# Kernel tuning notes

Hardware: AMD Instinct MI355X
Metric: run time of the kernel (lower is better)

Reference implementation:

```python
import jax, jax.numpy as jnp
import numpy as np
from jax import lax

N, L, D, F = 16, 512, 256, 256
KW = 3
EPS = 1e-5


def setup_inputs() -> dict:
    key = jax.random.key(0)
    ks = jax.random.split(key, 12)
    return {
        "x": jax.random.normal(ks[0], (N, L, D), jnp.float32),
        "conv1_w": jax.random.normal(ks[1], (F, D, KW), jnp.float32) * 0.05,
        "conv1_b": jnp.zeros((F,), jnp.float32),
        "ln1_g": jnp.ones((F,), jnp.float32),
        "ln1_b": jnp.zeros((F,), jnp.float32),
        "conv2_w": jax.random.normal(ks[2], (F, F, KW), jnp.float32) * 0.05,
        "conv2_b": jnp.zeros((F,), jnp.float32),
        "ln2_g": jnp.ones((F,), jnp.float32),
        "ln2_b": jnp.zeros((F,), jnp.float32),
        "lin_w": jax.random.normal(ks[3], (F, 1), jnp.float32) * 0.05,
        "lin_b": jnp.zeros((1,), jnp.float32),
        "target": jax.random.randint(ks[4], (N, L), 1, 8, jnp.int32),
        "mel_max_length": 4096,
    }


def _layernorm(h, g, b):
    m = jnp.mean(h, axis=-1, keepdims=True)
    v = jnp.var(h, axis=-1, keepdims=True)
    return (h - m) * lax.rsqrt(v + EPS) * g + b


def _conv1d(h, w, b):
    # h: [N, L, C_in]; w: [C_out, C_in, K]; 'same' padding=1 for K=3
    y = lax.conv_general_dilated(h.transpose(0, 2, 1), w, (1,), [(1, 1)],
                                 dimension_numbers=("NCH", "OIH", "NCH"))
    return (y + b[None, :, None]).transpose(0, 2, 1)


def _duration_predictor(x, c1w, c1b, g1, b1, c2w, c2b, g2, b2, lw, lb):
    h = jax.nn.relu(_layernorm(_conv1d(x, c1w, c1b), g1, b1))
    h = jax.nn.relu(_layernorm(_conv1d(h, c2w, c2b), g2, b2))
    return jax.nn.relu(h @ lw + lb)[..., 0]  # [N, L]


def _length_regulate(x, dur, T):
    # Equivalent to one-hot alignment @ x, done as a duration-indexed gather.
    cum = jnp.cumsum(dur, axis=-1)                       # [N, L]
    t = jnp.arange(T, dtype=cum.dtype)                   # [T]
    idx = jax.vmap(lambda c: jnp.searchsorted(c, t, side="right"))(cum)  # [N, T]
    valid = t[None, :] < cum[:, -1:]                     # [N, T]
    out = jnp.take_along_axis(x, jnp.clip(idx, 0, x.shape[1] - 1)[:, :, None], axis=1)
    return jnp.where(valid[..., None], out, jnp.zeros((), x.dtype))


def reference(x, conv1_w, conv1_b, ln1_g, ln1_b, conv2_w, conv2_b, ln2_g, ln2_b,
              lin_w, lin_b, target, mel_max_length):
    dpo = _duration_predictor(x, conv1_w, conv1_b, ln1_g, ln1_b,
                              conv2_w, conv2_b, ln2_g, ln2_b, lin_w, lin_b)
    out = _length_regulate(x, target, mel_max_length)    # [N, mel_max_length, D]
    return (out, dpo)
```

## Files before the change

kernel.cpp:

```cpp
#include <hip/hip_runtime.h>
#include <hip/hip_bf16.h>

using u16 = unsigned short;
typedef __bf16 bf16x8 __attribute__((ext_vector_type(8)));
typedef float f32x4 __attribute__((ext_vector_type(4)));

#define N_B   16
#define L_S   512
#define D_F   256
#define T_MEL 4096
#define M_TOT (N_B * L_S)
#define OUT_ELEMS ((size_t)N_B * T_MEL * D_F)
#define H1_ELEMS  ((size_t)M_TOT * D_F)
#define WP_ELEMS  (24 * 8192)
#define TBLK 128

__device__ __forceinline__ u16 f2bf(float f) {
  __hip_bfloat16 h = __float2bfloat16(f);
  return *(u16*)&h;
}

__device__ __forceinline__ bf16x8 pack8(float4 v0, float4 v1) {
  union { bf16x8 h; u16 u[8]; } r;
  r.u[0] = f2bf(v0.x); r.u[1] = f2bf(v0.y); r.u[2] = f2bf(v0.z); r.u[3] = f2bf(v0.w);
  r.u[4] = f2bf(v1.x); r.u[5] = f2bf(v1.y); r.u[6] = f2bf(v1.z); r.u[7] = f2bf(v1.w);
  return r.h;
}

__global__ __launch_bounds__(256)
void pack_kernel(const float* __restrict__ w1, const float* __restrict__ w2,
                 u16* __restrict__ wp1, u16* __restrict__ wp2) {
  int o   = (int)blockIdx.x * 256 + (int)threadIdx.x;
  int s   = o >> 13;
  int rem = o & 8191;
  int f   = rem >> 5;
  int ki  = rem & 31;
  int d   = ((s & 7) << 5) + ki;
  int tap = s >> 3;
  int src = f * 768 + d * 3 + tap;
  wp1[o] = f2bf(w1[src]);
  wp2[o] = f2bf(w2[src]);
}

template<int STAGE>
__global__ __launch_bounds__(512)
void conv_ln_kernel(const float* __restrict__ Xf,
                    const u16*  __restrict__ Xh,
                    const u16*  __restrict__ Wp,
                    const float* __restrict__ cb,  const float* __restrict__ lgm,
                    const float* __restrict__ lbt, const float* __restrict__ lw,
                    const float* __restrict__ lb,  u16* __restrict__ Hout,
                    float* __restrict__ dpo)
{
  __shared__ __align__(16) u16 As[34 * 264 + 8];
  __shared__ __align__(16) u16 Bs[2 * 8192];
  __shared__ float sBias[256], sG[256], sB[256], sLw[256];
  __shared__ float redS[2][4][16], redQ[2][4][16];

  const int t = threadIdx.x;
  if (t < 256) {
    sBias[t] = cb[t];
    sG[t]    = lgm[t];
    sB[t]    = lbt[t];
    if (STAGE == 2) sLw[t] = lw[t];
  }

  const int m0   = (int)blockIdx.x * 32;
  const int n    = m0 >> 9;
  const int l0   = m0 & 511;
  const int wave = t >> 6, lane = t & 63;
  const int cs   = wave & 3;
  const int rh   = wave >> 2;
  const int wc   = cs * 64;
  const int rh16 = rh * 16;
  const int p    = lane & 15, q = lane >> 4;

  for (int c = t; c < 1088; c += 512) {
    int row  = c >> 5;
    int col8 = c & 31;
    int l    = l0 + row - 1;
    uint4 val;
    if ((unsigned)l < 512u) {
      if (STAGE == 1) {
        const float* src = Xf + (((size_t)((n << 9) + l)) << 8) + (col8 << 3);
        float4 v0 = *(const float4*)src;
        float4 v1 = *(const float4*)(src + 4);
        bf16x8 pk = pack8(v0, v1);
        __builtin_memcpy(&val, &pk, 16);
      } else {
        val = *(const uint4*)(Xh + (((size_t)((n << 9) + l)) << 8) + (col8 << 3));
      }
    } else {
      val = make_uint4(0u, 0u, 0u, 0u);
    }
    *(uint4*)(As + row * 264 + (col8 << 3)) = val;
  }
  {
    uint4 r0 = *(const uint4*)(Wp + (t << 3));
    uint4 r1 = *(const uint4*)(Wp + ((t + 512) << 3));
    *(uint4*)(Bs + (t << 3))         = r0;
    *(uint4*)(Bs + ((t + 512) << 3)) = r1;
  }
  __syncthreads();

  f32x4 acc[4];
  #pragma unroll
  for (int i = 0; i < 4; i++) acc[i] = (f32x4){0.f, 0.f, 0.f, 0.f};

  for (int s = 0; s < 24; s++) {
    const int cur = s & 1;
    uint4 r0, r1;
    if (s < 23) {
      const u16* src = Wp + ((size_t)(s + 1) << 13);
      r0 = *(const uint4*)(src + (t << 3));
      r1 = *(const uint4*)(src + ((t + 512) << 3));
    }
    {
      const u16* bs = Bs + (cur << 13);
      const int tap = s >> 3, dbase = (s & 7) << 5;
      bf16x8 af = *(const bf16x8*)(As + (rh16 + p + tap) * 264 + dbase + (q << 3));
      #pragma unroll
      for (int ct = 0; ct < 4; ct++) {
        bf16x8 bfr = *(const bf16x8*)(bs + ((wc + ct * 16 + p) << 5) + (q << 3));
        acc[ct] = __builtin_amdgcn_mfma_f32_16x16x32_bf16(af, bfr, acc[ct], 0, 0, 0);
      }
    }
    if (s < 23) {
      __syncthreads();
      *(uint4*)(Bs + ((cur ^ 1) << 13) + (t << 3))         = r0;
      *(uint4*)(Bs + ((cur ^ 1) << 13) + ((t + 512) << 3)) = r1;
      __syncthreads();
    }
  }

  float s0[4] = {0,0,0,0}, s1[4] = {0,0,0,0};
  #pragma unroll
  for (int ct = 0; ct < 4; ct++) {
    float bias = sBias[wc + ct * 16 + p];
    #pragma unroll
    for (int j = 0; j < 4; j++) {
      float v = acc[ct][j] + bias;
      acc[ct][j] = v;
      s0[j] += v;
      s1[j] += v * v;
    }
  }
  #pragma unroll
  for (int m = 1; m <= 8; m <<= 1) {
    #pragma unroll
    for (int j = 0; j < 4; j++) {
      s0[j] += __shfl_xor(s0[j], m);
      s1[j] += __shfl_xor(s1[j], m);
    }
  }
  if (p == 0) {
    #pragma unroll
    for (int j = 0; j < 4; j++) {
      redS[rh][cs][q * 4 + j] = s0[j];
      redQ[rh][cs][q * 4 + j] = s1[j];
    }
  }
  __syncthreads();
  float mean[4], rstd[4];
  #pragma unroll
  for (int j = 0; j < 4; j++) {
    int r = q * 4 + j;
    float S = redS[rh][0][r] + redS[rh][1][r] + redS[rh][2][r] + redS[rh][3][r];
    float Q = redQ[rh][0][r] + redQ[rh][1][r] + redQ[rh][2][r] + redQ[rh][3][r];
    float mu  = S * (1.0f / 256.0f);
    float var = Q * (1.0f / 256.0f) - mu * mu;
    mean[j] = mu;
    rstd[j] = rsqrtf(var + 1e-5f);
  }

  if (STAGE == 1) {
    #pragma unroll
    for (int ct = 0; ct < 4; ct++) {
      int c = wc + ct * 16 + p;
      float gg = sG[c], bb = sB[c];
      #pragma unroll
      for (int j = 0; j < 4; j++) {
        float v = (acc[ct][j] - mean[j]) * rstd[j] * gg + bb;
        v = fmaxf(v, 0.0f);
        Hout[(size_t)(m0 + rh16 + q * 4 + j) * 256 + c] = f2bf(v);
      }
    }
  } else {
    float ls[4] = {0,0,0,0};
    #pragma unroll
    for (int ct = 0; ct < 4; ct++) {
      int c = wc + ct * 16 + p;
      float gg = sG[c], bb = sB[c], ww = sLw[c];
      #pragma unroll
      for (int j = 0; j < 4; j++) {
        float v = (acc[ct][j] - mean[j]) * rstd[j] * gg + bb;
        v = fmaxf(v, 0.0f);
        ls[j] += v * ww;
      }
    }
    #pragma unroll
    for (int m = 1; m <= 8; m <<= 1) {
      #pragma unroll
      for (int j = 0; j < 4; j++) ls[j] += __shfl_xor(ls[j], m);
    }
    __syncthreads();
    if (p == 0) {
      #pragma unroll
      for (int j = 0; j < 4; j++) redS[rh][cs][q * 4 + j] = ls[j];
    }
    __syncthreads();
    if (t < 32) {
      int r2 = t >> 4, ri = t & 15;
      float dv = fmaxf(redS[r2][0][ri] + redS[r2][1][ri] +
                       redS[r2][2][ri] + redS[r2][3][ri] + lb[0], 0.0f);
      dpo[m0 + t] = dv;
    }
  }
}

__global__ __launch_bounds__(256)
void lr_kernel(const float* __restrict__ X, const int* __restrict__ tgt,
               float* __restrict__ out) {
  __shared__ int c[L_S];
  __shared__ int sidx[TBLK];
  const int t  = threadIdx.x;
  const int n  = blockIdx.x >> 5;
  const int t0 = (blockIdx.x & 31) * TBLK;

  c[t]       = tgt[n * L_S + t];
  c[t + 256] = tgt[n * L_S + t + 256];
  __syncthreads();
  for (int off = 1; off < L_S; off <<= 1) {
    int v0 = (t >= off) ? c[t - off] : 0;
    int i1 = t + 256;
    int v1 = (i1 >= off) ? c[i1 - off] : 0;
    __syncthreads();
    c[t]  += v0;
    c[i1] += v1;
    __syncthreads();
  }
  const int total = c[L_S - 1];
  if (t < TBLK) {
    int tt = t0 + t;
    int lo = 0, hi = L_S;
    while (lo < hi) {
      int mid = (lo + hi) >> 1;
      if (c[mid] <= tt) lo = mid + 1; else hi = mid;
    }
    sidx[t] = (tt < total) ? lo : -1;
  }
  __syncthreads();

  #pragma unroll
  for (int i = 0; i < 32; i++) {
    int u   = t + i * 256;
    int dg  = u & 63;
    int tr  = u >> 6;
    int idx = sidx[tr];
    float4 v = make_float4(0.f, 0.f, 0.f, 0.f);
    if (idx >= 0)
      v = *(const float4*)(X + (((size_t)(n * L_S + idx)) << 8) + dg * 4);
    *(float4*)(out + (((size_t)(n * T_MEL + t0 + tr)) << 8) + dg * 4) = v;
  }
}

extern "C" void kernel_launch(void* const* d_in, const int* in_sizes, int n_in,
                              void* d_out, int out_size, void* d_ws, size_t ws_size,
                              hipStream_t stream) {
  (void)d_ws; (void)ws_size; (void)in_sizes; (void)n_in; (void)out_size;

  const float* x   = (const float*)d_in[0];
  const float* w1  = (const float*)d_in[1];
  const float* b1  = (const float*)d_in[2];
  const float* g1  = (const float*)d_in[3];
  const float* be1 = (const float*)d_in[4];
  const float* w2  = (const float*)d_in[5];
  const float* b2  = (const float*)d_in[6];
  const float* g2  = (const float*)d_in[7];
  const float* be2 = (const float*)d_in[8];
  const float* lw  = (const float*)d_in[9];
  const float* lb  = (const float*)d_in[10];
  const int*   tgt = (const int*)d_in[11];

  float* out = (float*)d_out;
  float* dpo = out + OUT_ELEMS;

  u16* h1  = (u16*)d_out;
  u16* wp1 = h1 + H1_ELEMS;
  u16* wp2 = wp1 + WP_ELEMS;

  pack_kernel<<<768, 256, 0, stream>>>(w1, w2, wp1, wp2);
  conv_ln_kernel<1><<<M_TOT / 32, 512, 0, stream>>>(
      x, nullptr, wp1, b1, g1, be1, nullptr, nullptr, h1, nullptr);
  conv_ln_kernel<2><<<M_TOT / 32, 512, 0, stream>>>(
      nullptr, h1, wp2, b2, g2, be2, lw, lb, nullptr, dpo);
  lr_kernel<<<N_B * (T_MEL / TBLK), 256, 0, stream>>>(x, tgt, out);
}
```

Measured before the change: 142.3 us.

## Fuse weight pack, both conv-LN stages and length regulation into cooperative kernel

Replaces four separate launches (weight packing, two conv+layernorm stages, length regulation) with one persistent cooperative kernel of 256 blocks. The phases are separated by grid-wide syncs. This removes per-launch overhead and inter-kernel gaps, and the length-regulation phase is remapped to 512-thread blocks each covering 256 output frames. The trade-offs are grid.sync cost, cooperative-launch constraints, and extra shared memory from the combined phases, which could affect occupancy.

```diff
diff --git a/kernel.cpp b/kernel.cpp
--- a/kernel.cpp
+++ b/kernel.cpp
@@ -1,5 +1,8 @@
 #include <hip/hip_runtime.h>
 #include <hip/hip_bf16.h>
+#include <hip/hip_cooperative_groups.h>
+
+namespace cg = cooperative_groups;
 
 using u16 = unsigned short;
 typedef __bf16 bf16x8 __attribute__((ext_vector_type(8)));
@@ -13,7 +16,6 @@
 #define OUT_ELEMS ((size_t)N_B * T_MEL * D_F)
 #define H1_ELEMS  ((size_t)M_TOT * D_F)
 #define WP_ELEMS  (24 * 8192)
-#define TBLK 128
 
 __device__ __forceinline__ u16 f2bf(float f) {
   __hip_bfloat16 h = __float2bfloat16(f);
@@ -27,37 +29,20 @@
   return r.h;
 }
 
-__global__ __launch_bounds__(256)
-void pack_kernel(const float* __restrict__ w1, const float* __restrict__ w2,
-                 u16* __restrict__ wp1, u16* __restrict__ wp2) {
-  int o   = (int)blockIdx.x * 256 + (int)threadIdx.x;
-  int s   = o >> 13;
-  int rem = o & 8191;
-  int f   = rem >> 5;
-  int ki  = rem & 31;
-  int d   = ((s & 7) << 5) + ki;
-  int tap = s >> 3;
-  int src = f * 768 + d * 3 + tap;
-  wp1[o] = f2bf(w1[src]);
-  wp2[o] = f2bf(w2[src]);
-}
-
 template<int STAGE>
-__global__ __launch_bounds__(512)
-void conv_ln_kernel(const float* __restrict__ Xf,
-                    const u16*  __restrict__ Xh,
-                    const u16*  __restrict__ Wp,
-                    const float* __restrict__ cb,  const float* __restrict__ lgm,
-                    const float* __restrict__ lbt, const float* __restrict__ lw,
-                    const float* __restrict__ lb,  u16* __restrict__ Hout,
-                    float* __restrict__ dpo)
+__device__ __forceinline__ void conv_phase(
+    const int blk, const int t,
+    const float* __restrict__ Xf,
+    const u16*  __restrict__ Xh,
+    const u16*  __restrict__ Wp,
+    const float* __restrict__ cb,  const float* __restrict__ lgm,
+    const float* __restrict__ lbt, const float* __restrict__ lw,
+    const float* __restrict__ lb,  u16* __restrict__ Hout,
+    float* __restrict__ dpo,
+    u16* As, u16* Bs,
+    float* sBias, float* sG, float* sB, float* sLw,
+    float (*redS)[4][16], float (*redQ)[4][16])
 {
-  __shared__ __align__(16) u16 As[34 * 264 + 8];
-  __shared__ __align__(16) u16 Bs[2 * 8192];
-  __shared__ float sBias[256], sG[256], sB[256], sLw[256];
-  __shared__ float redS[2][4][16], redQ[2][4][16];
-
-  const int t = threadIdx.x;
   if (t < 256) {
     sBias[t] = cb[t];
     sG[t]    = lgm[t];
@@ -65,7 +50,7 @@
     if (STAGE == 2) sLw[t] = lw[t];
   }
 
-  const int m0   = (int)blockIdx.x * 32;
+  const int m0   = blk * 32;
   const int n    = m0 >> 9;
   const int l0   = m0 & 511;
   const int wave = t >> 6, lane = t & 63;
@@ -218,49 +203,87 @@
   }
 }
 
-__global__ __launch_bounds__(256)
-void lr_kernel(const float* __restrict__ X, const int* __restrict__ tgt,
-               float* __restrict__ out) {
-  __shared__ int c[L_S];
-  __shared__ int sidx[TBLK];
-  const int t  = threadIdx.x;
-  const int n  = blockIdx.x >> 5;
-  const int t0 = (blockIdx.x & 31) * TBLK;
-
-  c[t]       = tgt[n * L_S + t];
-  c[t + 256] = tgt[n * L_S + t + 256];
-  __syncthreads();
-  for (int off = 1; off < L_S; off <<= 1) {
-    int v0 = (t >= off) ? c[t - off] : 0;
-    int i1 = t + 256;
-    int v1 = (i1 >= off) ? c[i1 - off] : 0;
+__global__ __launch_bounds__(512)
+void mega_kernel(const float* __restrict__ x,
+                 const float* __restrict__ w1, const float* __restrict__ b1,
+                 const float* __restrict__ g1, const float* __restrict__ be1,
+                 const float* __restrict__ w2, const float* __restrict__ b2,
+                 const float* __restrict__ g2, const float* __restrict__ be2,
+                 const float* __restrict__ lw, const float* __restrict__ lb,
+                 const int* __restrict__ tgt,
+                 float* out, float* dpo, u16* h1, u16* wp1, u16* wp2)
+{
+  cg::grid_group grid = cg::this_grid();
+
+  __shared__ __align__(16) u16 As[34 * 264 + 8];
+  __shared__ __align__(16) u16 Bs[2 * 8192];
+  __shared__ float sBias[256], sG[256], sB[256], sLw[256];
+  __shared__ float redS[2][4][16], redQ[2][4][16];
+  __shared__ int  sc[512];
+  __shared__ int  sidx[256];
+
+  const int t   = threadIdx.x;
+  const int blk = (int)blockIdx.x;
+
+  {
+    int gid = blk * 512 + t;
+    for (int o = gid; o < 196608; o += 131072) {
+      int s   = o >> 13;
+      int rem = o & 8191;
+      int f   = rem >> 5;
+      int ki  = rem & 31;
+      int d   = ((s & 7) << 5) + ki;
+      int tap = s >> 3;
+      int src = f * 768 + d * 3 + tap;
+      wp1[o] = f2bf(w1[src]);
+      wp2[o] = f2bf(w2[src]);
+    }
+  }
+  grid.sync();
+
+  conv_phase<1>(blk, t, x, nullptr, wp1, b1, g1, be1, nullptr, nullptr,
+                h1, nullptr, As, Bs, sBias, sG, sB, sLw, redS, redQ);
+  grid.sync();
+
+  conv_phase<2>(blk, t, nullptr, h1, wp2, b2, g2, be2, lw, lb,
+                nullptr, dpo, As, Bs, sBias, sG, sB, sLw, redS, redQ);
+  grid.sync();
+
+  {
+    const int n  = blk >> 4;
+    const int t0 = (blk & 15) * 256;
+
+    sc[t] = tgt[n * L_S + t];
     __syncthreads();
-    c[t]  += v0;
-    c[i1] += v1;
+    for (int off = 1; off < L_S; off <<= 1) {
+      int v = (t >= off) ? sc[t - off] : 0;
+      __syncthreads();
+      sc[t] += v;
+      __syncthreads();
+    }
+    const int total = sc[L_S - 1];
+    if (t < 256) {
+      int tt = t0 + t;
+      int lo = 0, hi = L_S;
+      while (lo < hi) {
+        int mid = (lo + hi) >> 1;
+        if (sc[mid] <= tt) lo = mid + 1; else hi = mid;
+      }
+      sidx[t] = (tt < total) ? lo : -1;
+    }
     __syncthreads();
-  }
-  const int total = c[L_S - 1];
-  if (t < TBLK) {
-    int tt = t0 + t;
-    int lo = 0, hi = L_S;
-    while (lo < hi) {
-      int mid = (lo + hi) >> 1;
-      if (c[mid] <= tt) lo = mid + 1; else hi = mid;
-    }
-    sidx[t] = (tt < total) ? lo : -1;
-  }
-  __syncthreads();
-
-  #pragma unroll
-  for (int i = 0; i < 32; i++) {
-    int u   = t + i * 256;
-    int dg  = u & 63;
-    int tr  = u >> 6;
-    int idx = sidx[tr];
-    float4 v = make_float4(0.f, 0.f, 0.f, 0.f);
-    if (idx >= 0)
-      v = *(const float4*)(X + (((size_t)(n * L_S + idx)) << 8) + dg * 4);
-    *(float4*)(out + (((size_t)(n * T_MEL + t0 + tr)) << 8) + dg * 4) = v;
+
+    #pragma unroll
+    for (int i = 0; i < 32; i++) {
+      int u   = t + i * 512;
+      int dg  = u & 63;
+      int tr  = u >> 6;
+      int idx = sidx[tr];
+      float4 v = make_float4(0.f, 0.f, 0.f, 0.f);
+      if (idx >= 0)
+        v = *(const float4*)(x + (((size_t)(n * L_S + idx)) << 8) + dg * 4);
+      *(float4*)(out + (((size_t)(n * T_MEL + t0 + tr)) << 8) + dg * 4) = v;
+    }
   }
 }
 
@@ -289,10 +312,12 @@
   u16* wp1 = h1 + H1_ELEMS;
   u16* wp2 = wp1 + WP_ELEMS;
 
-  pack_kernel<<<768, 256, 0, stream>>>(w1, w2, wp1, wp2);
-  conv_ln_kernel<1><<<M_TOT / 32, 512, 0, stream>>>(
-      x, nullptr, wp1, b1, g1, be1, nullptr, nullptr, h1, nullptr);
-  conv_ln_kernel<2><<<M_TOT / 32, 512, 0, stream>>>(
-      nullptr, h1, wp2, b2, g2, be2, lw, lb, nullptr, dpo);
-  lr_kernel<<<N_B * (T_MEL / TBLK), 256, 0, stream>>>(x, tgt, out);
-}
+  void* args[] = {
+    (void*)&x,  (void*)&w1, (void*)&b1, (void*)&g1, (void*)&be1,
+    (void*)&w2, (void*)&b2, (void*)&g2, (void*)&be2,
+    (void*)&lw, (void*)&lb, (void*)&tgt,
+    (void*)&out, (void*)&dpo, (void*)&h1, (void*)&wp1, (void*)&wp2
+  };
+  hipLaunchCooperativeKernel((const void*)mega_kernel, dim3(256), dim3(512),
+                             args, 0, stream);
+}
```

Measured after the change: 238.1 us. 67.3% more time.

## Co-schedule conv1 and length-regulate gather in one launch using workspace scratch

Applied to the files above, without the earlier changes.

Merges the first conv+LayerNorm stage and the length-regulation gather into a single kernel. Blocks 0-255 run conv1, and the remaining 256 blocks run a 512-thread length-regulate that covers 256 mel frames each. Scratch buffers (h1 and the packed weights) move from the output buffer into the workspace, which removes the ordering dependency that forced the gather to run last. The aim is to overlap the compute-bound conv with the bandwidth-bound gather and save one launch. In exchange, the fused kernel's shared-memory footprint applies to the gather blocks too, which may limit occupancy. The old path is kept as a fallback when no workspace is available.

```diff
diff --git a/kernel.cpp b/kernel.cpp
--- a/kernel.cpp
+++ b/kernel.cpp
@@ -43,21 +43,17 @@
 }
 
 template<int STAGE>
-__global__ __launch_bounds__(512)
-void conv_ln_kernel(const float* __restrict__ Xf,
-                    const u16*  __restrict__ Xh,
-                    const u16*  __restrict__ Wp,
-                    const float* __restrict__ cb,  const float* __restrict__ lgm,
-                    const float* __restrict__ lbt, const float* __restrict__ lw,
-                    const float* __restrict__ lb,  u16* __restrict__ Hout,
-                    float* __restrict__ dpo)
+__device__ __forceinline__ void conv_body(
+    const int blk, const int t,
+    const float* __restrict__ Xf, const u16* __restrict__ Xh,
+    const u16* __restrict__ Wp,
+    const float* __restrict__ cb,  const float* __restrict__ lgm,
+    const float* __restrict__ lbt, const float* __restrict__ lw,
+    const float* __restrict__ lb,  u16* __restrict__ Hout,
+    float* __restrict__ dpo,
+    u16* As, u16* Bs, float* sBias, float* sG, float* sB, float* sLw,
+    float (*redS)[4][16], float (*redQ)[4][16])
 {
-  __shared__ __align__(16) u16 As[34 * 264 + 8];
-  __shared__ __align__(16) u16 Bs[2 * 8192];
-  __shared__ float sBias[256], sG[256], sB[256], sLw[256];
-  __shared__ float redS[2][4][16], redQ[2][4][16];
-
-  const int t = threadIdx.x;
   if (t < 256) {
     sBias[t] = cb[t];
     sG[t]    = lgm[t];
@@ -65,7 +61,7 @@
     if (STAGE == 2) sLw[t] = lw[t];
   }
 
-  const int m0   = (int)blockIdx.x * 32;
+  const int m0   = blk * 32;
   const int n    = m0 >> 9;
   const int l0   = m0 & 511;
   const int wave = t >> 6, lane = t & 63;
@@ -218,6 +214,86 @@
   }
 }
 
+__device__ __forceinline__ void lr_body512(
+    const int lrblk, const int t,
+    const float* __restrict__ X, const int* __restrict__ tgt,
+    float* __restrict__ out, int* sc, int* sidx)
+{
+  const int n  = lrblk >> 4;
+  const int t0 = (lrblk & 15) * 256;
+
+  sc[t] = tgt[n * L_S + t];
+  __syncthreads();
+  for (int off = 1; off < L_S; off <<= 1) {
+    int v = (t >= off) ? sc[t - off] : 0;
+    __syncthreads();
+    sc[t] += v;
+    __syncthreads();
+  }
+  const int total = sc[L_S - 1];
+  if (t < 256) {
+    int tt = t0 + t;
+    int lo = 0, hi = L_S;
+    while (lo < hi) {
+      int mid = (lo + hi) >> 1;
+      if (sc[mid] <= tt) lo = mid + 1; else hi = mid;
+    }
+    sidx[t] = (tt < total) ? lo : -1;
+  }
+  __syncthreads();
+
+  #pragma unroll
+  for (int i = 0; i < 32; i++) {
+    int u   = t + i * 512;
+    int dg  = u & 63;
+    int tr  = u >> 6;
+    int idx = sidx[tr];
+    float4 v = make_float4(0.f, 0.f, 0.f, 0.f);
+    if (idx >= 0)
+      v = *(const float4*)(X + (((size_t)(n * L_S + idx)) << 8) + dg * 4);
+    *(float4*)(out + (((size_t)(n * T_MEL + t0 + tr)) << 8) + dg * 4) = v;
+  }
+}
+
+template<int STAGE>
+__global__ __launch_bounds__(512)
+void conv_ln_kernel(const float* __restrict__ Xf, const u16* __restrict__ Xh,
+                    const u16* __restrict__ Wp,
+                    const float* __restrict__ cb,  const float* __restrict__ lgm,
+                    const float* __restrict__ lbt, const float* __restrict__ lw,
+                    const float* __restrict__ lb,  u16* __restrict__ Hout,
+                    float* __restrict__ dpo)
+{
+  __shared__ __align__(16) u16 As[34 * 264 + 8];
+  __shared__ __align__(16) u16 Bs[2 * 8192];
+  __shared__ float sBias[256], sG[256], sB[256], sLw[256];
+  __shared__ float redS[2][4][16], redQ[2][4][16];
+  conv_body<STAGE>((int)blockIdx.x, (int)threadIdx.x, Xf, Xh, Wp, cb, lgm, lbt,
+                   lw, lb, Hout, dpo, As, Bs, sBias, sG, sB, sLw, redS, redQ);
+}
+
+__global__ __launch_bounds__(512)
+void conv1_lr_kernel(const float* __restrict__ x, const u16* __restrict__ Wp,
+                     const float* __restrict__ cb,  const float* __restrict__ lgm,
+                     const float* __restrict__ lbt, u16* __restrict__ Hout,
+                     const int* __restrict__ tgt, float* __restrict__ out)
+{
+  __shared__ __align__(16) u16 As[34 * 264 + 8];
+  __shared__ __align__(16) u16 Bs[2 * 8192];
+  __shared__ float sBias[256], sG[256], sB[256], sLw[256];
+  __shared__ float redS[2][4][16], redQ[2][4][16];
+  __shared__ int  sc[512];
+  __shared__ int  sidx[256];
+
+  const int blk = (int)blockIdx.x, t = (int)threadIdx.x;
+  if (blk < 256) {
+    conv_body<1>(blk, t, x, nullptr, Wp, cb, lgm, lbt, nullptr, nullptr,
+                 Hout, nullptr, As, Bs, sBias, sG, sB, sLw, redS, redQ);
+  } else {
+    lr_body512(blk - 256, t, x, tgt, out, sc, sidx);
+  }
+}
+
 __global__ __launch_bounds__(256)
 void lr_kernel(const float* __restrict__ X, const int* __restrict__ tgt,
                float* __restrict__ out) {
@@ -267,7 +343,7 @@
 extern "C" void kernel_launch(void* const* d_in, const int* in_sizes, int n_in,
                               void* d_out, int out_size, void* d_ws, size_t ws_size,
                               hipStream_t stream) {
-  (void)d_ws; (void)ws_size; (void)in_sizes; (void)n_in; (void)out_size;
+  (void)in_sizes; (void)n_in; (void)out_size;
 
   const float* x   = (const float*)d_in[0];
   const float* w1  = (const float*)d_in[1];
@@ -285,14 +361,25 @@
   float* out = (float*)d_out;
   float* dpo = out + OUT_ELEMS;
 
-  u16* h1  = (u16*)d_out;
-  u16* wp1 = h1 + H1_ELEMS;
-  u16* wp2 = wp1 + WP_ELEMS;
-
-  pack_kernel<<<768, 256, 0, stream>>>(w1, w2, wp1, wp2);
-  conv_ln_kernel<1><<<M_TOT / 32, 512, 0, stream>>>(
-      x, nullptr, wp1, b1, g1, be1, nullptr, nullptr, h1, nullptr);
-  conv_ln_kernel<2><<<M_TOT / 32, 512, 0, stream>>>(
-      nullptr, h1, wp2, b2, g2, be2, lw, lb, nullptr, dpo);
-  lr_kernel<<<N_B * (T_MEL / TBLK), 256, 0, stream>>>(x, tgt, out);
-}
+  const size_t need = (H1_ELEMS + 2 * (size_t)WP_ELEMS) * sizeof(u16);
+
+  if (d_ws != nullptr && ws_size >= need) {
+    u16* h1  = (u16*)d_ws;
+    u16* wp1 = h1 + H1_ELEMS;
+    u16* wp2 = wp1 + WP_ELEMS;
+    pack_kernel<<<768, 256, 0, stream>>>(w1, w2, wp1, wp2);
+    conv1_lr_kernel<<<512, 512, 0, stream>>>(x, wp1, b1, g1, be1, h1, tgt, out);
+    conv_ln_kernel<2><<<M_TOT / 32, 512, 0, stream>>>(
+        nullptr, h1, wp2, b2, g2, be2, lw, lb, nullptr, dpo);
+  } else {
+    u16* h1  = (u16*)d_out;
+    u16* wp1 = h1 + H1_ELEMS;
+    u16* wp2 = wp1 + WP_ELEMS;
+    pack_kernel<<<768, 256, 0, stream>>>(w1, w2, wp1, wp2);
+    conv_ln_kernel<1><<<M_TOT / 32, 512, 0, stream>>>(
+        x, nullptr, wp1, b1, g1, be1, nullptr, nullptr, h1, nullptr);
+    conv_ln_kernel<2><<<M_TOT / 32, 512, 0, stream>>>(
+        nullptr, h1, wp2, b2, g2, be2, lw, lb, nullptr, dpo);
+    lr_kernel<<<N_B * (T_MEL / TBLK), 256, 0, stream>>>(x, tgt, out);
+  }
+}
```

After: 128.5 us. 1.11x faster.
